# Performance work log

Hardware: AMD Instinct MI355X
Metric: run time of the kernel (lower is better)

## Reference

```python
import jax, jax.numpy as jnp
import numpy as np

B, S, D_IN, D_OUT = 8, 2048, 768, 768

def setup_inputs() -> dict:
    key = jax.random.key(0)
    k1, k2 = jax.random.split(key)
    x = jax.random.normal(k1, (B, S, D_IN), dtype=jnp.float32)
    QKV = jax.random.normal(k2, (3, D_IN, D_OUT), dtype=jnp.float32) * 0.02
    return {"x": x, "QKV": QKV}

def reference(x, QKV):
    # Single-head self-attention; scale uses sqrt(d_in) as in the original.
    q = jnp.einsum('bsd,de->bse', x, QKV[0])  # [B,S,D_OUT]
    k = jnp.einsum('bsd,de->bse', x, QKV[1])
    v = jnp.einsum('bsd,de->bse', x, QKV[2])
    scale = 1.0 / jnp.sqrt(jnp.asarray(x.shape[-1], dtype=x.dtype))
    scores = jnp.einsum('bqe,bke->bqk', q, k) * scale  # [B,S,S]
    probs = jax.nn.softmax(scores, axis=-1)
    return jnp.einsum('bqk,bke->bqe', probs, v)  # [B,S,D_OUT]
```

## Files before the change

### kernel.cpp

```cpp
#include <hip/hip_runtime.h>
#include <hip/hip_bf16.h>
#include <cstdint>


#define NB 8
#define NS 2048
#define ND 768
#define NQKV 2304
#define MTOT 16384

using f32x4 = __attribute__((ext_vector_type(4))) float;
using s16x8 = __attribute__((ext_vector_type(8))) short;

struct alignas(16) bf16x8 { __hip_bfloat16 h[8]; };
struct alignas(8)  bf16x4 { __hip_bfloat16 h[4]; };

__global__ __launch_bounds__(256) void convert_x_kernel(const float* __restrict__ x,
                                                        __hip_bfloat16* __restrict__ xb) {
    const int i = blockIdx.x * 256 + threadIdx.x;
    const float4 v = ((const float4*)x)[i];
    bf16x4 o;
    o.h[0] = __float2bfloat16(v.x);
    o.h[1] = __float2bfloat16(v.y);
    o.h[2] = __float2bfloat16(v.z);
    o.h[3] = __float2bfloat16(v.w);
    ((bf16x4*)xb)[i] = o;
}

__global__ __launch_bounds__(256) void transpose_w_kernel(const float* __restrict__ W,
                                                          __hip_bfloat16* __restrict__ Wt) {
    __shared__ float tile[32][33];
    const int e = blockIdx.z;
    const int k0 = blockIdx.y * 32, n0 = blockIdx.x * 32;
    const float* Wp = W + (size_t)e * ND * ND;
    __hip_bfloat16* Wo = Wt + (size_t)e * ND * ND;
    for (int r = threadIdx.y; r < 32; r += 8)
        tile[r][threadIdx.x] = Wp[(k0 + r) * ND + n0 + threadIdx.x];
    __syncthreads();
    for (int r = threadIdx.y; r < 32; r += 8)
        Wo[(long)(n0 + r) * ND + k0 + threadIdx.x] = __float2bfloat16(tile[threadIdx.x][r]);
}

__global__ __launch_bounds__(256) void transpose_v_kernel(const __hip_bfloat16* __restrict__ qkv,
                                                          __hip_bfloat16* __restrict__ vt) {
    __shared__ __hip_bfloat16 tile[32][33];
    const int b = blockIdx.z;
    const int s0 = blockIdx.y * 32, d0 = blockIdx.x * 32;
    for (int r = threadIdx.y; r < 32; r += 8)
        tile[r][threadIdx.x] = qkv[(long)(b * NS + s0 + r) * NQKV + 1536 + d0 + threadIdx.x];
    __syncthreads();
    for (int r = threadIdx.y; r < 32; r += 8)
        vt[((long)b * ND + d0 + r) * NS + s0 + threadIdx.x] = tile[threadIdx.x][r];
}

__device__ __forceinline__ void storeC(float* p, float v) { *p = v; }
__device__ __forceinline__ void storeC(__hip_bfloat16* p, float v) { *p = __float2bfloat16(v); }

template <typename OutT, bool BATCH_X>
__global__ __launch_bounds__(256, 3) void gemm_bt_kernel(
    const __hip_bfloat16* __restrict__ A,
    const __hip_bfloat16* __restrict__ Bm,
    OutT* __restrict__ C,
    int K, int lda, int ldb, int ldc,
    long sA, long sB, long sC, float scale) {
    __shared__ __hip_bfloat16 As[128 * 64];
    __shared__ __hip_bfloat16 Bs[128 * 64];

    int b, tileM, tileN;
    if (BATCH_X) {
        b = blockIdx.x; tileN = blockIdx.y * 128; tileM = blockIdx.z * 128;
    } else {
        b = blockIdx.z; tileN = blockIdx.x * 128; tileM = blockIdx.y * 128;
    }
    A  += (long)b * sA;
    Bm += (long)b * sB;
    C  += (long)b * sC;

    const int tid  = threadIdx.x;
    const int lane = tid & 63;
    const int wave = tid >> 6;
    const int wm = (wave >> 1) * 64;
    const int wn = (wave & 1) * 64;
    const int quad = lane >> 4;
    const int lrow = lane & 15;

    const int srow = tid >> 3;
    const int schunk = (tid & 7) ^ (srow & 7);
    const int scol = schunk << 3;

    f32x4 acc[4][4];
    const f32x4 zero = {0.f, 0.f, 0.f, 0.f};
#pragma unroll
    for (int i = 0; i < 4; ++i)
#pragma unroll
        for (int j = 0; j < 4; ++j) acc[i][j] = zero;

    const __hip_bfloat16* gA = A + (long)(tileM + srow) * lda + scol;
    const __hip_bfloat16* gB = Bm + (long)(tileN + srow) * ldb + scol;
    char* AsB = (char*)As;
    char* BsB = (char*)Bs;
    const int ldsOff = tid * 16;

    typedef const __attribute__((address_space(1))) void* gp;
    typedef __attribute__((address_space(3))) void* sp;

    const int swa = (lrow & 7) << 4;

    for (int k0 = 0; k0 < K; k0 += 64) {
        __syncthreads();
#pragma unroll
        for (int j = 0; j < 4; ++j)
            __builtin_amdgcn_global_load_lds((gp)(gA + (long)(j * 32) * lda + k0),
                                             (sp)(AsB + j * 4096 + ldsOff), 16, 0, 0);
#pragma unroll
        for (int j = 0; j < 4; ++j)
            __builtin_amdgcn_global_load_lds((gp)(gB + (long)(j * 32) * ldb + k0),
                                             (sp)(BsB + j * 4096 + ldsOff), 16, 0, 0);
        __syncthreads();

#pragma unroll
        for (int kk = 0; kk < 2; ++kk) {
            s16x8 af[4], bfr[4];
#pragma unroll
            for (int i = 0; i < 4; ++i)
                af[i] = *(const s16x8*)(AsB + (wm + i * 16 + lrow) * 128 +
                                        ((((kk << 2) | quad) << 4) ^ swa));
#pragma unroll
            for (int j = 0; j < 4; ++j)
                bfr[j] = *(const s16x8*)(BsB + (wn + j * 16 + lrow) * 128 +
                                         ((((kk << 2) | quad) << 4) ^ swa));
#pragma unroll
            for (int i = 0; i < 4; ++i)
#pragma unroll
                for (int j = 0; j < 4; ++j)
                    acc[i][j] = __builtin_amdgcn_mfma_f32_16x16x32_bf16(af[i], bfr[j], acc[i][j], 0, 0, 0);
        }
    }

#pragma unroll
    for (int i = 0; i < 4; ++i) {
#pragma unroll
        for (int j = 0; j < 4; ++j) {
            const int col = tileN + wn + j * 16 + lrow;
#pragma unroll
            for (int r = 0; r < 4; ++r) {
                const int row = tileM + wm + i * 16 + quad * 4 + r;
                storeC(C + (long)row * ldc + col, acc[i][j][r] * scale);
            }
        }
    }
}

__global__ __launch_bounds__(256) void softmax_kernel(__hip_bfloat16* __restrict__ P) {
    const long row = (long)blockIdx.x * 4 + (threadIdx.x >> 6);
    const int lane = threadIdx.x & 63;
    __hip_bfloat16* p = P + row * NS;

    bf16x8 raw[4];
    float v[32];
#pragma unroll
    for (int c = 0; c < 4; ++c) raw[c] = *(const bf16x8*)(p + c * 512 + lane * 8);
#pragma unroll
    for (int c = 0; c < 4; ++c)
#pragma unroll
        for (int i = 0; i < 8; ++i) v[c * 8 + i] = __bfloat162float(raw[c].h[i]);

    float m = v[0];
#pragma unroll
    for (int i = 1; i < 32; ++i) m = fmaxf(m, v[i]);
#pragma unroll
    for (int off = 1; off < 64; off <<= 1) m = fmaxf(m, __shfl_xor(m, off));

    float s = 0.f;
#pragma unroll
    for (int i = 0; i < 32; ++i) {
        v[i] = __expf(v[i] - m);
        s += v[i];
    }
#pragma unroll
    for (int off = 1; off < 64; off <<= 1) s += __shfl_xor(s, off);
    const float inv = 1.f / s;

#pragma unroll
    for (int c = 0; c < 4; ++c) {
        bf16x8 o;
#pragma unroll
        for (int i = 0; i < 8; ++i) o.h[i] = __float2bfloat16(v[c * 8 + i] * inv);
        *(bf16x8*)(p + c * 512 + lane * 8) = o;
    }
}

extern "C" void kernel_launch(void* const* d_in, const int* in_sizes, int n_in,
                              void* d_out, int out_size, void* d_ws, size_t ws_size,
                              hipStream_t stream) {
    const float* x   = (const float*)d_in[0];
    const float* QKV = (const float*)d_in[1];
    float* out = (float*)d_out;

    uint8_t* ws = (uint8_t*)d_ws;
    constexpr size_t XB_BYTES  = (size_t)MTOT * ND * 2;
    constexpr size_t WT_BYTES  = (size_t)3 * ND * ND * 2;
    constexpr size_t QKV_BYTES = (size_t)MTOT * NQKV * 2;
    constexpr size_t VT_BYTES  = (size_t)NB * ND * NS * 2;
    __hip_bfloat16* xb    = (__hip_bfloat16*)(ws);
    __hip_bfloat16* Wt    = (__hip_bfloat16*)(ws + XB_BYTES);
    __hip_bfloat16* qkvb  = (__hip_bfloat16*)(ws + XB_BYTES + WT_BYTES);
    __hip_bfloat16* vt    = (__hip_bfloat16*)(ws + XB_BYTES + WT_BYTES + QKV_BYTES);
    __hip_bfloat16* probs = (__hip_bfloat16*)(ws + XB_BYTES + WT_BYTES + QKV_BYTES + VT_BYTES);

    const float scale = 0.03608439182435161f;

    convert_x_kernel<<<MTOT * ND / 1024, 256, 0, stream>>>(x, xb);
    transpose_w_kernel<<<dim3(ND / 32, ND / 32, 3), dim3(32, 8), 0, stream>>>(QKV, Wt);
    gemm_bt_kernel<__hip_bfloat16, false><<<dim3(NQKV / 128, MTOT / 128, 1), 256, 0, stream>>>(
        xb, Wt, qkvb, ND, ND, ND, NQKV, 0, 0, 0, 1.0f);
    transpose_v_kernel<<<dim3(ND / 32, NS / 32, NB), dim3(32, 8), 0, stream>>>(qkvb, vt);
    gemm_bt_kernel<__hip_bfloat16, true><<<dim3(NB, NS / 128, NS / 128), 256, 0, stream>>>(
        qkvb, qkvb + 768, probs, ND, NQKV, NQKV, NS,
        (long)NS * NQKV, (long)NS * NQKV, (long)NS * NS, scale);
    softmax_kernel<<<MTOT / 4, 256, 0, stream>>>(probs);
    gemm_bt_kernel<float, true><<<dim3(NB, ND / 128, NS / 128), 256, 0, stream>>>(
        probs, vt, out, NS, NS, NS, ND,
        (long)NS * NS, (long)ND * NS, (long)NS * ND, 1.0f);
}
```

Before: 313.9 us.

## Fuse V transpose into QKV GEMM epilogue and merge preprocessing kernels

The QKV projection GEMM now writes V tiles transposed straight into the vt buffer through an LDS-staged, swizzled epilogue, so Q/K are stored with a narrower 1536 stride and the separate V transpose kernel is dropped. The x conversion and weight transpose are merged into one launch. This removes one kernel launch and the full write-plus-reread of V through global memory. In exchange the epilogue adds extra LDS traffic and barriers in the V blocks.

```diff
diff --git a/kernel.cpp b/kernel.cpp
--- a/kernel.cpp
+++ b/kernel.cpp
@@ -6,7 +6,7 @@
 #define NB 8
 #define NS 2048
 #define ND 768
-#define NQKV 2304
+#define NQK 1536
 #define MTOT 16384
 
 using f32x4 = __attribute__((ext_vector_type(4))) float;
@@ -15,56 +15,51 @@
 struct alignas(16) bf16x8 { __hip_bfloat16 h[8]; };
 struct alignas(8)  bf16x4 { __hip_bfloat16 h[4]; };
 
-__global__ __launch_bounds__(256) void convert_x_kernel(const float* __restrict__ x,
-                                                        __hip_bfloat16* __restrict__ xb) {
-    const int i = blockIdx.x * 256 + threadIdx.x;
-    const float4 v = ((const float4*)x)[i];
-    bf16x4 o;
-    o.h[0] = __float2bfloat16(v.x);
-    o.h[1] = __float2bfloat16(v.y);
-    o.h[2] = __float2bfloat16(v.z);
-    o.h[3] = __float2bfloat16(v.w);
-    ((bf16x4*)xb)[i] = o;
-}
-
-__global__ __launch_bounds__(256) void transpose_w_kernel(const float* __restrict__ W,
-                                                          __hip_bfloat16* __restrict__ Wt) {
+#define CVT_BLOCKS 12288
+__global__ __launch_bounds__(256) void preprocess_kernel(const float* __restrict__ x,
+                                                         __hip_bfloat16* __restrict__ xb,
+                                                         const float* __restrict__ W,
+                                                         __hip_bfloat16* __restrict__ Wt) {
     __shared__ float tile[32][33];
-    const int e = blockIdx.z;
-    const int k0 = blockIdx.y * 32, n0 = blockIdx.x * 32;
-    const float* Wp = W + (size_t)e * ND * ND;
-    __hip_bfloat16* Wo = Wt + (size_t)e * ND * ND;
-    for (int r = threadIdx.y; r < 32; r += 8)
-        tile[r][threadIdx.x] = Wp[(k0 + r) * ND + n0 + threadIdx.x];
-    __syncthreads();
-    for (int r = threadIdx.y; r < 32; r += 8)
-        Wo[(long)(n0 + r) * ND + k0 + threadIdx.x] = __float2bfloat16(tile[threadIdx.x][r]);
-}
-
-__global__ __launch_bounds__(256) void transpose_v_kernel(const __hip_bfloat16* __restrict__ qkv,
-                                                          __hip_bfloat16* __restrict__ vt) {
-    __shared__ __hip_bfloat16 tile[32][33];
-    const int b = blockIdx.z;
-    const int s0 = blockIdx.y * 32, d0 = blockIdx.x * 32;
-    for (int r = threadIdx.y; r < 32; r += 8)
-        tile[r][threadIdx.x] = qkv[(long)(b * NS + s0 + r) * NQKV + 1536 + d0 + threadIdx.x];
-    __syncthreads();
-    for (int r = threadIdx.y; r < 32; r += 8)
-        vt[((long)b * ND + d0 + r) * NS + s0 + threadIdx.x] = tile[threadIdx.x][r];
+    const int tid = threadIdx.x;
+    if (blockIdx.x < CVT_BLOCKS) {
+        const int i = blockIdx.x * 256 + tid;
+        const float4 v = ((const float4*)x)[i];
+        bf16x4 o;
+        o.h[0] = __float2bfloat16(v.x);
+        o.h[1] = __float2bfloat16(v.y);
+        o.h[2] = __float2bfloat16(v.z);
+        o.h[3] = __float2bfloat16(v.w);
+        ((bf16x4*)xb)[i] = o;
+    } else {
+        const int bid = blockIdx.x - CVT_BLOCKS;
+        const int e = bid / 576, rem = bid % 576;
+        const int k0 = (rem / 24) * 32, n0 = (rem % 24) * 32;
+        const int tx = tid & 31, ty = tid >> 5;
+        const float* Wp = W + (size_t)e * ND * ND;
+        __hip_bfloat16* Wo = Wt + (size_t)e * ND * ND;
+        for (int r = ty; r < 32; r += 8)
+            tile[r][tx] = Wp[(k0 + r) * ND + n0 + tx];
+        __syncthreads();
+        for (int r = ty; r < 32; r += 8)
+            Wo[(long)(n0 + r) * ND + k0 + tx] = __float2bfloat16(tile[tx][r]);
+    }
 }
 
 __device__ __forceinline__ void storeC(float* p, float v) { *p = v; }
 __device__ __forceinline__ void storeC(__hip_bfloat16* p, float v) { *p = __float2bfloat16(v); }
 
-template <typename OutT, bool BATCH_X>
+template <typename OutT, int EPI, bool BATCH_X>
 __global__ __launch_bounds__(256, 3) void gemm_bt_kernel(
     const __hip_bfloat16* __restrict__ A,
     const __hip_bfloat16* __restrict__ Bm,
     OutT* __restrict__ C,
+    __hip_bfloat16* __restrict__ vtOut,
     int K, int lda, int ldb, int ldc,
     long sA, long sB, long sC, float scale) {
-    __shared__ __hip_bfloat16 As[128 * 64];
-    __shared__ __hip_bfloat16 Bs[128 * 64];
+    __shared__ char smem[32768];
+    char* AsB = smem;
+    char* BsB = smem + 16384;
 
     int b, tileM, tileN;
     if (BATCH_X) {
@@ -97,8 +92,6 @@
 
     const __hip_bfloat16* gA = A + (long)(tileM + srow) * lda + scol;
     const __hip_bfloat16* gB = Bm + (long)(tileN + srow) * ldb + scol;
-    char* AsB = (char*)As;
-    char* BsB = (char*)Bs;
     const int ldsOff = tid * 16;
 
     typedef const __attribute__((address_space(1))) void* gp;
@@ -135,6 +128,38 @@
                 for (int j = 0; j < 4; ++j)
                     acc[i][j] = __builtin_amdgcn_mfma_f32_16x16x32_bf16(af[i], bfr[j], acc[i][j], 0, 0, 0);
         }
+    }
+
+    if (EPI == 2 && tileN >= NQK) {
+        __syncthreads();
+        char* T = smem;
+#pragma unroll
+        for (int i = 0; i < 4; ++i) {
+#pragma unroll
+            for (int j = 0; j < 4; ++j) {
+                const int d = wn + j * 16 + lrow;
+                const int s = wm + i * 16 + quad * 4;
+                bf16x4 g;
+#pragma unroll
+                for (int r = 0; r < 4; ++r) g.h[r] = __float2bfloat16(acc[i][j][r]);
+                const int c = s >> 3;
+                const int off = d * 256 + (((c ^ (d & 15)) << 4) | ((s & 4) << 1));
+                *(bf16x4*)(T + off) = g;
+            }
+        }
+        __syncthreads();
+        const int dl = tid >> 1, half = tid & 1;
+        const long bb = tileM >> 11;
+        const int s0 = tileM & (NS - 1);
+        const long dg = (long)(tileN - NQK) + dl;
+        __hip_bfloat16* dst = vtOut + (bb * ND + dg) * NS + s0;
+#pragma unroll
+        for (int cc = 0; cc < 8; ++cc) {
+            const int c2 = half * 8 + cc;
+            s16x8 val = *(const s16x8*)(T + dl * 256 + ((c2 ^ (dl & 15)) << 4));
+            *(s16x8*)(dst + c2 * 8) = val;
+        }
+        return;
     }
 
 #pragma unroll
@@ -200,7 +225,7 @@
     uint8_t* ws = (uint8_t*)d_ws;
     constexpr size_t XB_BYTES  = (size_t)MTOT * ND * 2;
     constexpr size_t WT_BYTES  = (size_t)3 * ND * ND * 2;
-    constexpr size_t QKV_BYTES = (size_t)MTOT * NQKV * 2;
+    constexpr size_t QKV_BYTES = (size_t)MTOT * NQK * 2;
     constexpr size_t VT_BYTES  = (size_t)NB * ND * NS * 2;
     __hip_bfloat16* xb    = (__hip_bfloat16*)(ws);
     __hip_bfloat16* Wt    = (__hip_bfloat16*)(ws + XB_BYTES);
@@ -210,16 +235,14 @@
 
     const float scale = 0.03608439182435161f;
 
-    convert_x_kernel<<<MTOT * ND / 1024, 256, 0, stream>>>(x, xb);
-    transpose_w_kernel<<<dim3(ND / 32, ND / 32, 3), dim3(32, 8), 0, stream>>>(QKV, Wt);
-    gemm_bt_kernel<__hip_bfloat16, false><<<dim3(NQKV / 128, MTOT / 128, 1), 256, 0, stream>>>(
-        xb, Wt, qkvb, ND, ND, ND, NQKV, 0, 0, 0, 1.0f);
-    transpose_v_kernel<<<dim3(ND / 32, NS / 32, NB), dim3(32, 8), 0, stream>>>(qkvb, vt);
-    gemm_bt_kernel<__hip_bfloat16, true><<<dim3(NB, NS / 128, NS / 128), 256, 0, stream>>>(
-        qkvb, qkvb + 768, probs, ND, NQKV, NQKV, NS,
-        (long)NS * NQKV, (long)NS * NQKV, (long)NS * NS, scale);
+    preprocess_kernel<<<CVT_BLOCKS + 1728, 256, 0, stream>>>(x, xb, QKV, Wt);
+    gemm_bt_kernel<__hip_bfloat16, 2, false><<<dim3(2304 / 128, MTOT / 128, 1), 256, 0, stream>>>(
+        xb, Wt, qkvb, vt, ND, ND, ND, NQK, 0, 0, 0, 1.0f);
+    gemm_bt_kernel<__hip_bfloat16, 0, true><<<dim3(NB, NS / 128, NS / 128), 256, 0, stream>>>(
+        qkvb, qkvb + ND, probs, nullptr, ND, NQK, NQK, NS,
+        (long)NS * NQK, (long)NS * NQK, (long)NS * NS, scale);
     softmax_kernel<<<MTOT / 4, 256, 0, stream>>>(probs);
-    gemm_bt_kernel<float, true><<<dim3(NB, ND / 128, NS / 128), 256, 0, stream>>>(
-        probs, vt, out, NS, NS, NS, ND,
+    gemm_bt_kernel<float, 1, true><<<dim3(NB, ND / 128, NS / 128), 256, 0, stream>>>(
+        probs, vt, out, nullptr, NS, NS, NS, ND,
         (long)NS * NS, (long)ND * NS, (long)NS * ND, 1.0f);
 }
```

Result: faster. 289.3 us (-7.8%).
